# Optimization experiments

Measured on AMD Instinct MI355X. Metric: run time of the kernel, lower is better.

Reference implementation:

```python
import jax, jax.numpy as jnp
import numpy as np

RADIUS = 400.0
FIELD = 8000.0  # um extent of slide coordinate field


def setup_inputs() -> dict:
    key = jax.random.key(0)
    ks = jax.random.split(key, 8)
    B, N, D, H, K = 4, 4096, 1536, 512, 8
    images = jax.random.normal(ks[0], (B, N, D), dtype=jnp.float32)
    positions = jax.random.uniform(ks[1], (B, N, 2), dtype=jnp.float32) * FIELD
    W_feat = jax.random.normal(ks[2], (D, H), dtype=jnp.float32) * (1.0 / np.sqrt(D))
    b_feat = jnp.zeros((H,), dtype=jnp.float32)
    W_pos = jax.random.normal(ks[3], (2, H), dtype=jnp.float32) * 0.5
    W_gnn = jax.random.normal(ks[4], (H, H), dtype=jnp.float32) * (1.0 / np.sqrt(H))
    W_self = jax.random.normal(ks[5], (H, H), dtype=jnp.float32) * (1.0 / np.sqrt(H))
    anchors = jax.random.normal(ks[6], (K, D), dtype=jnp.float32)
    return {"images": images, "positions": positions, "W_feat": W_feat,
            "b_feat": b_feat, "W_pos": W_pos, "W_gnn": W_gnn,
            "W_self": W_self, "anchors": anchors}


def _radius_adjacency(pos):
    # pos: (N, 2). Dense O(N^2) radius graph (mirrors torch.cdist + mask).
    sq = jnp.sum(pos * pos, axis=-1)                       # (N,)
    d2 = sq[:, None] + sq[None, :] - 2.0 * (pos @ pos.T)   # (N, N)
    mask = d2 < (RADIUS * RADIUS)
    N = pos.shape[0]
    mask = mask & ~jnp.eye(N, dtype=bool)                  # no self-loops
    return mask.astype(pos.dtype)


def reference(images, positions, W_feat, b_feat, W_pos, W_gnn, W_self, anchors):
    # --- Stream A: explicit concept quantifier (cosine sim to anchors) ---
    x_norm = images / jnp.clip(jnp.linalg.norm(images, axis=-1, keepdims=True), 1e-12)
    a_norm = anchors / jnp.clip(jnp.linalg.norm(anchors, axis=-1, keepdims=True), 1e-12)
    scores = jnp.einsum('bnd,kd->bnk', x_norm, a_norm)     # (B, N, K)
    concept_profile = scores.mean(axis=1)                  # (B, K)

    # --- Stream B: feature extraction with positional encoding ---
    feat = images @ W_feat + b_feat + positions @ W_pos    # (B, N, H)

    # --- radius graph + one mean-aggregation GNN layer, per slide ---
    def per_graph(f, p):
        A = _radius_adjacency(p)                           # (N, N)
        deg = jnp.clip(A.sum(axis=-1, keepdims=True), 1.0) # (N, 1)
        h = jax.nn.relu(f)
        agg = (A @ h) / deg                                # mean over neighbors
        return jax.nn.relu(agg @ W_gnn + f @ W_self)       # (N, H)

    refined = jax.vmap(per_graph)(feat, positions)         # (B, N, H)
    latent_spatial = refined.mean(axis=1)                  # (B, H)  per-graph mean pool

    return jnp.concatenate([latent_spatial, concept_profile], axis=1)  # (B, H+K)
```

## Files before the change

kernel.cpp:

```cpp
#include <hip/hip_runtime.h>

#define B_ 4
#define N_ 4096
#define D_ 1536
#define H_ 512
#define K_ 8
#define M_ (B_*N_)
#define R2_ 160000.0f
#define CAP 192

typedef __attribute__((ext_vector_type(8))) short bf16x8;
typedef __attribute__((ext_vector_type(4))) float f32x4;
typedef __attribute__((ext_vector_type(2))) float f32x2;

__device__ __forceinline__ unsigned short f2bf(float f) {
  union { float f; unsigned u; } v; v.f = f;
  unsigned r = (v.u + 0x7FFFu + ((v.u >> 16) & 1u)) >> 16;
  return (unsigned short)r;
}

typedef const __attribute__((address_space(1))) unsigned int gas_u32;
typedef __attribute__((address_space(3))) unsigned int las_u32;
__device__ __forceinline__ void gl_lds16(const unsigned short* g, unsigned short* l) {
  __builtin_amdgcn_global_load_lds((gas_u32*)g, (las_u32*)l, 16, 0, 0);
}

__global__ __launch_bounds__(256) void k_prep(
    const float* __restrict__ Wf, const float* __restrict__ Wg, const float* __restrict__ Ws,
    const float* __restrict__ anchors, unsigned short* __restrict__ WfT,
    unsigned short* __restrict__ WgsT, float* __restrict__ anorm) {
  __shared__ float t[64][65];
  __shared__ float red[4];
  int bx = blockIdx.x, by = blockIdx.y, tid = threadIdx.x;
  if (by == 40) {
    int k = bx;
    float s = 0.f;
    for (int i = tid; i < D_; i += 256) { float v = anchors[k*D_ + i]; s += v*v; }
    #pragma unroll
    for (int off = 32; off; off >>= 1) s += __shfl_down(s, off);
    if ((tid & 63) == 0) red[tid >> 6] = s;
    __syncthreads();
    if (tid == 0) anorm[k] = fmaxf(sqrtf(red[0]+red[1]+red[2]+red[3]), 1e-12f);
    return;
  }
  const float* W; unsigned short* WT; int kt, outStride, outOff;
  if (by < 24)      { W = Wf; WT = WfT;  kt = by;      outStride = D_;   outOff = 0; }
  else if (by < 32) { W = Wg; WT = WgsT; kt = by - 24; outStride = 1024; outOff = 0; }
  else              { W = Ws; WT = WgsT; kt = by - 32; outStride = 1024; outOff = 512; }
  int tx = tid & 63, ty = tid >> 6;
  #pragma unroll
  for (int r = 0; r < 64; r += 4)
    t[ty + r][tx] = W[(size_t)(kt*64 + ty + r)*H_ + bx*64 + tx];
  __syncthreads();
  #pragma unroll
  for (int r = 0; r < 64; r += 4) {
    int n = bx*64 + ty + r;
    WT[(size_t)n*outStride + outOff + kt*64 + tx] = f2bf(t[tx][ty + r]);
  }
}

__global__ __launch_bounds__(256) void k_concept_cast(
    const float* __restrict__ images, const float* __restrict__ anchors,
    const float* __restrict__ anorm, unsigned short* __restrict__ imgs_bf,
    float* __restrict__ out) {
  __shared__ float sA[K_*D_];
  __shared__ float sc[4][K_];
  int tid = threadIdx.x, lane = tid & 63, w = tid >> 6;
  {
    const float4* a4 = (const float4*)anchors;
    float4* sA4 = (float4*)sA;
    #pragma unroll
    for (int i = 0; i < 12; i++) sA4[tid + 256*i] = a4[tid + 256*i];
  }
  __syncthreads();
  float acc_k[K_] = {};
  for (int r = 0; r < 8; r++) {
    int gm = blockIdx.x*32 + w*8 + r;
    const float4* xrow = (const float4*)(images + (size_t)gm*D_);
    float nrm = 0.f; float dot[K_] = {};
    #pragma unroll
    for (int it = 0; it < 6; it++) {
      int j = lane + 64*it;
      float4 x = xrow[j];
      nrm += x.x*x.x + x.y*x.y + x.z*x.z + x.w*x.w;
      #pragma unroll
      for (int k = 0; k < K_; k++) {
        float4 a = *(const float4*)&sA[(size_t)(k*384 + j)*4];
        dot[k] += x.x*a.x + x.y*a.y + x.z*a.z + x.w*a.w;
      }
      ushort4 s;
      s.x = f2bf(x.x); s.y = f2bf(x.y); s.z = f2bf(x.z); s.w = f2bf(x.w);
      *(ushort4*)&imgs_bf[(size_t)gm*D_ + (size_t)j*4] = s;
    }
    #pragma unroll
    for (int off = 32; off; off >>= 1) {
      nrm += __shfl_down(nrm, off);
      #pragma unroll
      for (int k = 0; k < K_; k++) dot[k] += __shfl_down(dot[k], off);
    }
    if (lane == 0) {
      float inv = 1.0f / fmaxf(sqrtf(nrm), 1e-12f);
      #pragma unroll
      for (int k = 0; k < K_; k++) acc_k[k] += dot[k] * inv / anorm[k];
    }
  }
  if (lane == 0) {
    #pragma unroll
    for (int k = 0; k < K_; k++) sc[w][k] = acc_k[k];
  }
  __syncthreads();
  if (tid < K_) {
    float s = sc[0][tid] + sc[1][tid] + sc[2][tid] + sc[3][tid];
    int b = blockIdx.x >> 7;
    atomicAdd(out + b*(H_+K_) + H_ + tid, s * (1.0f/N_));
  }
}

#define BM 128
#define BN 128
#define BK 32

__global__ __launch_bounds__(256) void k_gemm(
    const unsigned short* __restrict__ A, const unsigned short* __restrict__ BT,
    int Kdim, int mode, const float* __restrict__ bias, const float* __restrict__ Wpos,
    const float* __restrict__ positions, unsigned short* __restrict__ AB,
    float* __restrict__ out) {
  __shared__ unsigned short As[BM*BK];
  __shared__ unsigned short Bs[BN*BK];
  __shared__ float colsum[BN];
  int tid = threadIdx.x;
  int lane = tid & 63, wv = tid >> 6;
  int wm = wv >> 1, wn = wv & 1;
  int l15 = lane & 15, quad = lane >> 4;
  int bx = blockIdx.x;
  int bm = bx >> 2, bn = bx & 3;
  int m0 = bm*BM, n0 = bn*BN;

  f32x4 acc[4][4] = {};

  int c = wv*2;
  int rowc = (lane >> 2), seg = lane & 3;
  const unsigned short* gA0 = A  + (size_t)(m0 + c*16 + rowc)*Kdim + seg*8;
  const unsigned short* gA1 = gA0 + (size_t)16*Kdim;
  const unsigned short* gB0 = BT + (size_t)(n0 + c*16 + rowc)*Kdim + seg*8;
  const unsigned short* gB1 = gB0 + (size_t)16*Kdim;
  unsigned short* lA0 = As + c*512;
  unsigned short* lA1 = lA0 + 512;
  unsigned short* lB0 = Bs + c*512;
  unsigned short* lB1 = lB0 + 512;

  int nk = Kdim / BK;
  for (int kt = 0; kt < nk; kt++) {
    __syncthreads();
    gl_lds16(gA0, lA0); gl_lds16(gA1, lA1);
    gl_lds16(gB0, lB0); gl_lds16(gB1, lB1);
    gA0 += BK; gA1 += BK; gB0 += BK; gB1 += BK;
    __syncthreads();

    bf16x8 aF[4], bF[4];
    #pragma unroll
    for (int f = 0; f < 4; f++)
      aF[f] = *(const bf16x8*)&As[(wm*64 + f*16 + l15)*BK + quad*8];
    #pragma unroll
    for (int f = 0; f < 4; f++)
      bF[f] = *(const bf16x8*)&Bs[(wn*64 + f*16 + l15)*BK + quad*8];
    #pragma unroll
    for (int mi = 0; mi < 4; mi++)
      #pragma unroll
      for (int ni = 0; ni < 4; ni++)
        acc[mi][ni] = __builtin_amdgcn_mfma_f32_16x16x32_bf16(aF[mi], bF[ni], acc[mi][ni], 0, 0, 0);
  }

  if (mode == 0) {
    float bz[4], w0v[4], w1v[4];
    #pragma unroll
    for (int ni = 0; ni < 4; ni++) {
      int gh = n0 + wn*64 + ni*16 + l15;
      bz[ni] = bias[gh]; w0v[ni] = Wpos[gh]; w1v[ni] = Wpos[H_ + gh];
    }
    #pragma unroll
    for (int mi = 0; mi < 4; mi++) {
      #pragma unroll
      for (int r = 0; r < 4; r++) {
        int gm = m0 + wm*64 + mi*16 + quad*4 + r;
        float2 p = ((const float2*)positions)[gm];
        #pragma unroll
        for (int ni = 0; ni < 4; ni++) {
          int gh = n0 + wn*64 + ni*16 + l15;
          float v = acc[mi][ni][r] + bz[ni] + p.x*w0v[ni] + p.y*w1v[ni];
          AB[(size_t)gm*1024 + 512 + gh] = f2bf(v);
        }
      }
    }
  } else {
    if (tid < BN) colsum[tid] = 0.f;
    __syncthreads();
    #pragma unroll
    for (int ni = 0; ni < 4; ni++) {
      float s = 0.f;
      #pragma unroll
      for (int mi = 0; mi < 4; mi++) {
        #pragma unroll
        for (int r = 0; r < 4; r++) s += fmaxf(acc[mi][ni][r], 0.f);
      }
      s += __shfl_down(s, 32);
      s += __shfl_down(s, 16);
      if (quad == 0) atomicAdd(&colsum[wn*64 + ni*16 + l15], s);
    }
    __syncthreads();
    if (tid < BN) {
      int b = m0 >> 12;
      atomicAdd(out + b*(H_+K_) + n0 + tid, colsum[tid] * (1.0f/N_));
    }
  }
}

__global__ __launch_bounds__(256) void k_quant(const unsigned short* __restrict__ AB,
                                               unsigned char* __restrict__ P) {
  int g = blockIdx.x*256 + threadIdx.x;
  int row = g >> 6, cg = (g & 63)*8;
  uint4 v = *(const uint4*)(AB + (size_t)row*1024 + 512 + cg);
  float f[8];
  union { unsigned u; float x; } t;
  t.u = v.x << 16; f[0]=t.x; t.u = v.x & 0xFFFF0000u; f[1]=t.x;
  t.u = v.y << 16; f[2]=t.x; t.u = v.y & 0xFFFF0000u; f[3]=t.x;
  t.u = v.z << 16; f[4]=t.x; t.u = v.z & 0xFFFF0000u; f[5]=t.x;
  t.u = v.w << 16; f[6]=t.x; t.u = v.w & 0xFFFF0000u; f[7]=t.x;
  #pragma unroll
  for (int i = 0; i < 8; i++) f[i] = fminf(fmaxf(f[i], 0.f)*0.015625f, 448.f);
  int u0 = __builtin_amdgcn_cvt_pk_fp8_f32(f[0], f[1], 0, false);
  u0     = __builtin_amdgcn_cvt_pk_fp8_f32(f[2], f[3], u0, true);
  int u1 = __builtin_amdgcn_cvt_pk_fp8_f32(f[4], f[5], 0, false);
  u1     = __builtin_amdgcn_cvt_pk_fp8_f32(f[6], f[7], u1, true);
  uint2 o; o.x = (unsigned)u0; o.y = (unsigned)u1;
  *(uint2*)(P + (size_t)row*512 + cg) = o;
}

__device__ __forceinline__ void accf8(uint2 v, float* a) {
  f32x2 p;
  p = __builtin_amdgcn_cvt_pk_f32_fp8(v.x, false); a[0] += p[0]; a[1] += p[1];
  p = __builtin_amdgcn_cvt_pk_f32_fp8(v.x, true);  a[2] += p[0]; a[3] += p[1];
  p = __builtin_amdgcn_cvt_pk_f32_fp8(v.y, false); a[4] += p[0]; a[5] += p[1];
  p = __builtin_amdgcn_cvt_pk_f32_fp8(v.y, true);  a[6] += p[0]; a[7] += p[1];
}

__global__ __launch_bounds__(256) void k_aggregate(const float* __restrict__ positions,
                                                   const unsigned char* __restrict__ P,
                                                   unsigned short* __restrict__ AB) {
  __shared__ unsigned short nl[8*CAP];
  __shared__ int cnt[8];
  __shared__ float sdx[8], sdy[8];
  int blk = blockIdx.x;
  int xcd = blk & 7;
  int b = xcd >> 1;
  int sub = ((blk >> 3) << 1) | (xcd & 1);
  int dest0 = sub * 8;
  int tid = threadIdx.x, lane = tid & 63, w = tid >> 6;
  const float2* p2 = (const float2*)(positions + (size_t)b*N_*2);
  if (tid < 8) {
    cnt[tid] = 0;
    float2 pd = p2[dest0 + tid];
    sdx[tid] = pd.x; sdy[tid] = pd.y;
  }
  __syncthreads();
  for (int it = 0; it < 16; it++) {
    int j = tid + 256*it;
    float2 pj = p2[j];
    #pragma unroll
    for (int d = 0; d < 8; d++) {
      float dx = pj.x - sdx[d], dy = pj.y - sdy[d];
      if (dx*dx + dy*dy < R2_ && j != dest0 + d) {
        int p = atomicAdd(&cnt[d], 1);
        if (p < CAP) nl[d*CAP + p] = (unsigned short)j;
      }
    }
  }
  __syncthreads();
  const unsigned char* featb = P + ((size_t)(b << 12))*512 + lane*8;
  #pragma unroll
  for (int dd = 0; dd < 2; dd++) {
    int d = w*2 + dd;
    int deg = cnt[d]; if (deg > CAP) deg = CAP;
    float inv = 64.0f / (float)(deg > 1 ? deg : 1);
    const unsigned short* nlp = &nl[d*CAP];
    float a[8] = {};
    int n = 0;
    for (; n + 4 <= deg; n += 4) {
      ushort4 idx = *(const ushort4*)&nlp[n];
      uint2 v0 = *(const uint2*)(featb + (size_t)idx.x*512);
      uint2 v1 = *(const uint2*)(featb + (size_t)idx.y*512);
      uint2 v2 = *(const uint2*)(featb + (size_t)idx.z*512);
      uint2 v3 = *(const uint2*)(featb + (size_t)idx.w*512);
      accf8(v0, a); accf8(v1, a); accf8(v2, a); accf8(v3, a);
    }
    for (; n < deg; n++) {
      int j = nlp[n];
      uint2 v = *(const uint2*)(featb + (size_t)j*512);
      accf8(v, a);
    }
    uint4 o;
    o.x = ((unsigned)f2bf(a[1]*inv) << 16) | f2bf(a[0]*inv);
    o.y = ((unsigned)f2bf(a[3]*inv) << 16) | f2bf(a[2]*inv);
    o.z = ((unsigned)f2bf(a[5]*inv) << 16) | f2bf(a[4]*inv);
    o.w = ((unsigned)f2bf(a[7]*inv) << 16) | f2bf(a[6]*inv);
    *(uint4*)(AB + (size_t)((b << 12) + dest0 + d)*1024 + lane*8) = o;
  }
}

extern "C" void kernel_launch(void* const* d_in, const int* in_sizes, int n_in,
                              void* d_out, int out_size, void* d_ws, size_t ws_size,
                              hipStream_t stream) {
  const float* images    = (const float*)d_in[0];
  const float* positions = (const float*)d_in[1];
  const float* W_feat    = (const float*)d_in[2];
  const float* b_feat    = (const float*)d_in[3];
  const float* W_pos     = (const float*)d_in[4];
  const float* W_gnn     = (const float*)d_in[5];
  const float* W_self    = (const float*)d_in[6];
  const float* anchors   = (const float*)d_in[7];
  float* out = (float*)d_out;

  char* ws = (char*)d_ws;
  unsigned short* imgs_bf = (unsigned short*)ws;
  unsigned char*  P       = (unsigned char*)ws;
  unsigned short* AB      = (unsigned short*)(ws + 50331648);
  unsigned short* WfT     = (unsigned short*)(ws + 83886080);
  unsigned short* WgsT    = (unsigned short*)(ws + 85458944);
  float*          anorm   = (float*)(ws + 86507520);

  hipMemsetAsync(d_out, 0, sizeof(float)*B_*(H_+K_), stream);
  k_prep<<<dim3(8, 41), 256, 0, stream>>>(W_feat, W_gnn, W_self, anchors, WfT, WgsT, anorm);
  k_concept_cast<<<M_/32, 256, 0, stream>>>(images, anchors, anorm, imgs_bf, out);
  k_gemm<<<512, 256, 0, stream>>>(imgs_bf, WfT, D_, 0, b_feat, W_pos, positions, AB, out);
  k_quant<<<4096, 256, 0, stream>>>(AB, P);
  k_aggregate<<<2048, 256, 0, stream>>>(positions, P, AB);
  k_gemm<<<512, 256, 0, stream>>>(AB, WgsT, 1024, 1, nullptr, nullptr, nullptr, AB, out);
}
```

Baseline: 290.5 us.

## Move anchor cosine scores into the feature GEMM as an extra MFMA column tile

The fp32 anchor dot products leave the cast kernel. The cast kernel now only converts images to bf16 and stores per-row inverse norms. Normalized anchors are packed into a zero-padded bf16 tile, and the first GEMM gets a fifth column block per row tile that computes the scores with MFMA and reduces them into the output. This strips the LDS-heavy scalar dot loop from the cast pass, at the cost of bf16 precision on the scores and extra GEMM blocks that reload the A tiles.

```diff
diff --git a/kernel.cpp b/kernel.cpp
--- a/kernel.cpp
+++ b/kernel.cpp
@@ -59,61 +59,39 @@
   }
 }
 
-__global__ __launch_bounds__(256) void k_concept_cast(
-    const float* __restrict__ images, const float* __restrict__ anchors,
-    const float* __restrict__ anorm, unsigned short* __restrict__ imgs_bf,
-    float* __restrict__ out) {
-  __shared__ float sA[K_*D_];
-  __shared__ float sc[4][K_];
-  int tid = threadIdx.x, lane = tid & 63, w = tid >> 6;
-  {
-    const float4* a4 = (const float4*)anchors;
-    float4* sA4 = (float4*)sA;
-    #pragma unroll
-    for (int i = 0; i < 12; i++) sA4[tid + 256*i] = a4[tid + 256*i];
-  }
-  __syncthreads();
-  float acc_k[K_] = {};
-  for (int r = 0; r < 8; r++) {
-    int gm = blockIdx.x*32 + w*8 + r;
-    const float4* xrow = (const float4*)(images + (size_t)gm*D_);
-    float nrm = 0.f; float dot[K_] = {};
-    #pragma unroll
-    for (int it = 0; it < 6; it++) {
-      int j = lane + 64*it;
-      float4 x = xrow[j];
-      nrm += x.x*x.x + x.y*x.y + x.z*x.z + x.w*x.w;
-      #pragma unroll
-      for (int k = 0; k < K_; k++) {
-        float4 a = *(const float4*)&sA[(size_t)(k*384 + j)*4];
-        dot[k] += x.x*a.x + x.y*a.y + x.z*a.z + x.w*a.w;
-      }
-      ushort4 s;
-      s.x = f2bf(x.x); s.y = f2bf(x.y); s.z = f2bf(x.z); s.w = f2bf(x.w);
-      *(ushort4*)&imgs_bf[(size_t)gm*D_ + (size_t)j*4] = s;
-    }
-    #pragma unroll
-    for (int off = 32; off; off >>= 1) {
-      nrm += __shfl_down(nrm, off);
-      #pragma unroll
-      for (int k = 0; k < K_; k++) dot[k] += __shfl_down(dot[k], off);
-    }
-    if (lane == 0) {
-      float inv = 1.0f / fmaxf(sqrtf(nrm), 1e-12f);
-      #pragma unroll
-      for (int k = 0; k < K_; k++) acc_k[k] += dot[k] * inv / anorm[k];
-    }
-  }
-  if (lane == 0) {
-    #pragma unroll
-    for (int k = 0; k < K_; k++) sc[w][k] = acc_k[k];
-  }
-  __syncthreads();
-  if (tid < K_) {
-    float s = sc[0][tid] + sc[1][tid] + sc[2][tid] + sc[3][tid];
-    int b = blockIdx.x >> 7;
-    atomicAdd(out + b*(H_+K_) + H_ + tid, s * (1.0f/N_));
-  }
+__global__ __launch_bounds__(256) void k_anch(const float* __restrict__ anchors,
+                                              const float* __restrict__ anorm,
+                                              unsigned short* __restrict__ AnchT) {
+  int t4 = blockIdx.x*256 + threadIdx.x;
+  int row = t4 / 384, c4 = t4 - row*384;
+  ushort4 s = {0,0,0,0};
+  if (row < 8) {
+    float inv = 1.0f / anorm[row];
+    float4 a = ((const float4*)anchors)[row*384 + c4];
+    s.x = f2bf(a.x*inv); s.y = f2bf(a.y*inv); s.z = f2bf(a.z*inv); s.w = f2bf(a.w*inv);
+  }
+  ((ushort4*)AnchT)[t4] = s;
+}
+
+__global__ __launch_bounds__(256) void k_cast(const float* __restrict__ images,
+                                              unsigned short* __restrict__ imgs_bf,
+                                              float* __restrict__ invn) {
+  int gm = blockIdx.x*4 + (threadIdx.x >> 6);
+  int lane = threadIdx.x & 63;
+  const float4* xrow = (const float4*)(images + (size_t)gm*D_);
+  float ss = 0.f;
+  #pragma unroll
+  for (int it = 0; it < 6; it++) {
+    int j = lane + 64*it;
+    float4 x = xrow[j];
+    ss += x.x*x.x + x.y*x.y + x.z*x.z + x.w*x.w;
+    ushort4 s;
+    s.x = f2bf(x.x); s.y = f2bf(x.y); s.z = f2bf(x.z); s.w = f2bf(x.w);
+    *(ushort4*)&imgs_bf[(size_t)gm*D_ + (size_t)j*4] = s;
+  }
+  #pragma unroll
+  for (int off = 32; off; off >>= 1) ss += __shfl_down(ss, off);
+  if (lane == 0) invn[gm] = 1.0f / fmaxf(sqrtf(ss), 1e-12f);
 }
 
 #define BM 128
@@ -123,7 +101,8 @@
 __global__ __launch_bounds__(256) void k_gemm(
     const unsigned short* __restrict__ A, const unsigned short* __restrict__ BT,
     int Kdim, int mode, const float* __restrict__ bias, const float* __restrict__ Wpos,
-    const float* __restrict__ positions, unsigned short* __restrict__ AB,
+    const float* __restrict__ positions, const unsigned short* __restrict__ AnchT,
+    const float* __restrict__ invn, unsigned short* __restrict__ AB,
     float* __restrict__ out) {
   __shared__ unsigned short As[BM*BK];
   __shared__ unsigned short Bs[BN*BK];
@@ -133,62 +112,98 @@
   int wm = wv >> 1, wn = wv & 1;
   int l15 = lane & 15, quad = lane >> 4;
   int bx = blockIdx.x;
-  int bm = bx >> 2, bn = bx & 3;
+  int bm, bn;
+  if (mode == 0) { bm = bx/5; bn = bx - bm*5; }
+  else           { bm = bx >> 2; bn = bx & 3; }
+  bool isC = (mode == 0) && (bn == 4);
   int m0 = bm*BM, n0 = bn*BN;
 
   f32x4 acc[4][4] = {};
 
   int c = wv*2;
   int rowc = (lane >> 2), seg = lane & 3;
-  const unsigned short* gA0 = A  + (size_t)(m0 + c*16 + rowc)*Kdim + seg*8;
+  const unsigned short* gA0 = A + (size_t)(m0 + c*16 + rowc)*Kdim + seg*8;
   const unsigned short* gA1 = gA0 + (size_t)16*Kdim;
-  const unsigned short* gB0 = BT + (size_t)(n0 + c*16 + rowc)*Kdim + seg*8;
+  const unsigned short* gB0;
+  if (isC) gB0 = AnchT + (size_t)rowc*Kdim + seg*8;
+  else     gB0 = BT + (size_t)(n0 + c*16 + rowc)*Kdim + seg*8;
   const unsigned short* gB1 = gB0 + (size_t)16*Kdim;
   unsigned short* lA0 = As + c*512;
   unsigned short* lA1 = lA0 + 512;
-  unsigned short* lB0 = Bs + c*512;
+  unsigned short* lB0 = isC ? Bs : Bs + c*512;
   unsigned short* lB1 = lB0 + 512;
 
   int nk = Kdim / BK;
   for (int kt = 0; kt < nk; kt++) {
     __syncthreads();
     gl_lds16(gA0, lA0); gl_lds16(gA1, lA1);
-    gl_lds16(gB0, lB0); gl_lds16(gB1, lB1);
+    if (!isC) { gl_lds16(gB0, lB0); gl_lds16(gB1, lB1); }
+    else if (wv == 0) gl_lds16(gB0, lB0);
     gA0 += BK; gA1 += BK; gB0 += BK; gB1 += BK;
     __syncthreads();
 
-    bf16x8 aF[4], bF[4];
+    bf16x8 aF[4];
     #pragma unroll
     for (int f = 0; f < 4; f++)
       aF[f] = *(const bf16x8*)&As[(wm*64 + f*16 + l15)*BK + quad*8];
-    #pragma unroll
-    for (int f = 0; f < 4; f++)
-      bF[f] = *(const bf16x8*)&Bs[(wn*64 + f*16 + l15)*BK + quad*8];
-    #pragma unroll
-    for (int mi = 0; mi < 4; mi++)
-      #pragma unroll
-      for (int ni = 0; ni < 4; ni++)
-        acc[mi][ni] = __builtin_amdgcn_mfma_f32_16x16x32_bf16(aF[mi], bF[ni], acc[mi][ni], 0, 0, 0);
+    if (isC) {
+      bf16x8 b0 = *(const bf16x8*)&Bs[l15*BK + quad*8];
+      #pragma unroll
+      for (int mi = 0; mi < 4; mi++)
+        acc[mi][0] = __builtin_amdgcn_mfma_f32_16x16x32_bf16(aF[mi], b0, acc[mi][0], 0, 0, 0);
+    } else {
+      bf16x8 bF[4];
+      #pragma unroll
+      for (int f = 0; f < 4; f++)
+        bF[f] = *(const bf16x8*)&Bs[(wn*64 + f*16 + l15)*BK + quad*8];
+      #pragma unroll
+      for (int mi = 0; mi < 4; mi++)
+        #pragma unroll
+        for (int ni = 0; ni < 4; ni++)
+          acc[mi][ni] = __builtin_amdgcn_mfma_f32_16x16x32_bf16(aF[mi], bF[ni], acc[mi][ni], 0, 0, 0);
+    }
   }
 
   if (mode == 0) {
-    float bz[4], w0v[4], w1v[4];
-    #pragma unroll
-    for (int ni = 0; ni < 4; ni++) {
-      int gh = n0 + wn*64 + ni*16 + l15;
-      bz[ni] = bias[gh]; w0v[ni] = Wpos[gh]; w1v[ni] = Wpos[H_ + gh];
-    }
-    #pragma unroll
-    for (int mi = 0; mi < 4; mi++) {
-      #pragma unroll
-      for (int r = 0; r < 4; r++) {
-        int gm = m0 + wm*64 + mi*16 + quad*4 + r;
-        float2 p = ((const float2*)positions)[gm];
+    if (isC) {
+      if (tid < 16) colsum[tid] = 0.f;
+      __syncthreads();
+      if (wn == 0) {
+        float part = 0.f;
         #pragma unroll
-        for (int ni = 0; ni < 4; ni++) {
-          int gh = n0 + wn*64 + ni*16 + l15;
-          float v = acc[mi][ni][r] + bz[ni] + p.x*w0v[ni] + p.y*w1v[ni];
-          AB[(size_t)gm*1024 + 512 + gh] = f2bf(v);
+        for (int mi = 0; mi < 4; mi++) {
+          #pragma unroll
+          for (int r = 0; r < 4; r++) {
+            int row = m0 + wm*64 + mi*16 + quad*4 + r;
+            part += acc[mi][0][r] * invn[row];
+          }
+        }
+        part += __shfl_down(part, 32);
+        part += __shfl_down(part, 16);
+        if (quad == 0) atomicAdd(&colsum[l15], part);
+      }
+      __syncthreads();
+      if (tid < 8)
+        atomicAdd(out + (m0 >> 12)*(H_+K_) + H_ + tid, colsum[tid] * (1.0f/N_));
+    } else {
+      float bz[4], w0v[4], w1v[4];
+      #pragma unroll
+      for (int ni = 0; ni < 4; ni++) {
+        int gh = n0 + wn*64 + ni*16 + l15;
+        bz[ni] = bias[gh]; w0v[ni] = Wpos[gh]; w1v[ni] = Wpos[H_ + gh];
+      }
+      #pragma unroll
+      for (int mi = 0; mi < 4; mi++) {
+        #pragma unroll
+        for (int r = 0; r < 4; r++) {
+          int gm = m0 + wm*64 + mi*16 + quad*4 + r;
+          float2 p = ((const float2*)positions)[gm];
+          #pragma unroll
+          for (int ni = 0; ni < 4; ni++) {
+            int gh = n0 + wn*64 + ni*16 + l15;
+            float v = acc[mi][ni][r] + bz[ni] + p.x*w0v[ni] + p.y*w1v[ni];
+            AB[(size_t)gm*1024 + 512 + gh] = f2bf(v);
+          }
         }
       }
     }
@@ -327,12 +342,15 @@
   unsigned short* WfT     = (unsigned short*)(ws + 83886080);
   unsigned short* WgsT    = (unsigned short*)(ws + 85458944);
   float*          anorm   = (float*)(ws + 86507520);
+  float*          invn    = (float*)(ws + 86508032);
+  unsigned short* AnchT   = (unsigned short*)(ws + 86573568);
 
   hipMemsetAsync(d_out, 0, sizeof(float)*B_*(H_+K_), stream);
   k_prep<<<dim3(8, 41), 256, 0, stream>>>(W_feat, W_gnn, W_self, anchors, WfT, WgsT, anorm);
-  k_concept_cast<<<M_/32, 256, 0, stream>>>(images, anchors, anorm, imgs_bf, out);
-  k_gemm<<<512, 256, 0, stream>>>(imgs_bf, WfT, D_, 0, b_feat, W_pos, positions, AB, out);
+  k_anch<<<24, 256, 0, stream>>>(anchors, anorm, AnchT);
+  k_cast<<<4096, 256, 0, stream>>>(images, imgs_bf, invn);
+  k_gemm<<<640, 256, 0, stream>>>(imgs_bf, WfT, D_, 0, b_feat, W_pos, positions, AnchT, invn, AB, out);
   k_quant<<<4096, 256, 0, stream>>>(AB, P);
   k_aggregate<<<2048, 256, 0, stream>>>(positions, P, AB);
-  k_gemm<<<512, 256, 0, stream>>>(AB, WgsT, 1024, 1, nullptr, nullptr, nullptr, AB, out);
-}
+  k_gemm<<<512, 256, 0, stream>>>(AB, WgsT, 1024, 1, nullptr, nullptr, nullptr, AnchT, invn, AB, out);
+}
```

Measured after the change: 347.7 us. +19.7%, slower.
